# Kernel tuning notes

Hardware: AMD Instinct MI355X
Metric: run time of the kernel (lower is better)

## Reference

```python
import jax, jax.numpy as jnp
import numpy as np

WS = 7  # window size
NH = 3  # num heads
EPS = 1e-5


def _rel_index(ws):
    coords = np.stack(np.meshgrid(np.arange(ws), np.arange(ws), indexing='ij'))  # [2,ws,ws]
    cf = coords.reshape(2, -1)  # [2, ws*ws]
    rel = cf[:, :, None] - cf[:, None, :]  # [2, N, N]
    rel = rel.transpose(1, 2, 0)
    rel[..., 0] += ws - 1
    rel[..., 1] += ws - 1
    rel[..., 0] *= 2 * ws - 1
    return rel.sum(-1).astype(np.int32)  # [N, N]


def setup_inputs() -> dict:
    key = jax.random.key(0)
    ks = jax.random.split(key, 8)
    dim, nh, ws = 96, NH, WS
    hid = 4 * dim
    s = 0.02
    inp = {
        'x': jax.random.normal(ks[0], (16, dim, 224, 224), jnp.float32),
        'ln1_g': jnp.ones((dim,), jnp.float32),
        'ln1_b': jnp.zeros((dim,), jnp.float32),
        'qkv_w': jax.random.normal(ks[1], (dim, 3 * dim), jnp.float32) * s,
        'qkv_b': jnp.zeros((3 * dim,), jnp.float32),
        'rpb_table': jax.random.normal(ks[2], ((2 * ws - 1) ** 2, nh), jnp.float32) * s,
        'proj_w': jax.random.normal(ks[3], (dim, dim), jnp.float32) * s,
        'proj_b': jnp.zeros((dim,), jnp.float32),
        'ln2_g': jnp.ones((dim,), jnp.float32),
        'ln2_b': jnp.zeros((dim,), jnp.float32),
        'mlp_w1': jax.random.normal(ks[4], (dim, hid), jnp.float32) * s,
        'mlp_b1': jnp.zeros((hid,), jnp.float32),
        'mlp_w2': jax.random.normal(ks[5], (hid, dim), jnp.float32) * s,
        'mlp_b2': jnp.zeros((dim,), jnp.float32),
        'rel_index': jnp.asarray(_rel_index(ws)),
    }
    return inp


def _layernorm(x, g, b):
    mu = jnp.mean(x, axis=-1, keepdims=True)
    var = jnp.mean(jnp.square(x - mu), axis=-1, keepdims=True)
    return (x - mu) * jax.lax.rsqrt(var + EPS) * g + b


def reference(x, ln1_g, ln1_b, qkv_w, qkv_b, rpb_table, proj_w, proj_b,
              ln2_g, ln2_b, mlp_w1, mlp_b1, mlp_w2, mlp_b2, rel_index):
    B, C, H, W = x.shape
    ws = WS
    pad_h = (ws - H % ws) % ws
    pad_w = (ws - W % ws) % ws
    x = jnp.transpose(x, (0, 2, 3, 1))  # BHWC
    if pad_h or pad_w:
        x = jnp.pad(x, ((0, 0), (0, pad_h), (0, pad_w), (0, 0)))
    Hp, Wp = H + pad_h, W + pad_w
    shortcut = x
    xn = _layernorm(x, ln1_g, ln1_b)

    # window partition -> [B*nW, N, C]
    N = ws * ws
    xw = xn.reshape(B, Hp // ws, ws, Wp // ws, ws, C)
    xw = jnp.transpose(xw, (0, 1, 3, 2, 4, 5)).reshape(-1, N, C)

    nh = NH
    hd = C // nh
    scale = hd ** -0.5
    qkv = xw @ qkv_w + qkv_b  # [Bw, N, 3C]
    qkv = qkv.reshape(-1, N, 3, nh, hd)
    qkv = jnp.transpose(qkv, (2, 0, 3, 1, 4))  # [3, Bw, nh, N, hd]
    q, k, v = qkv[0], qkv[1], qkv[2]
    attn = jnp.einsum('bhnd,bhmd->bhnm', q * scale, k)
    bias = rpb_table[rel_index.reshape(-1)].reshape(N, N, nh)  # gather
    attn = attn + jnp.transpose(bias, (2, 0, 1))[None]
    attn = jax.nn.softmax(attn, axis=-1)
    out = jnp.einsum('bhnm,bhmd->bhnd', attn, v)
    out = jnp.transpose(out, (0, 2, 1, 3)).reshape(-1, N, C)
    out = out @ proj_w + proj_b

    # window reverse
    xr = out.reshape(B, Hp // ws, Wp // ws, ws, ws, C)
    xr = jnp.transpose(xr, (0, 1, 3, 2, 4, 5)).reshape(B, Hp, Wp, C)

    x = shortcut + xr
    h = _layernorm(x, ln2_g, ln2_b)
    h = jax.nn.gelu(h @ mlp_w1 + mlp_b1, approximate=False) @ mlp_w2 + mlp_b2
    x = x + h
    x = jnp.transpose(x, (0, 3, 1, 2))  # BCHW
    if pad_h or pad_w:
        x = x[:, :, :H, :W]
    return x
```

## Files before the change

### kernel.cpp

```cpp
#include <hip/hip_runtime.h>
#include <math.h>

constexpr int C96  = 96;
constexpr int HW   = 50176;
constexpr int W224 = 224;
constexpr int QKVN = 288;
constexpr int HID  = 384;

typedef __bf16 bf16x8 __attribute__((ext_vector_type(8)));
typedef float  f32x4  __attribute__((ext_vector_type(4)));
typedef unsigned short u16x8 __attribute__((ext_vector_type(8)));

__device__ __forceinline__ float bf2f(unsigned short u) {
    return __uint_as_float(((unsigned int)u) << 16);
}
__device__ __forceinline__ unsigned short f2bf(float f) {
    unsigned int u = __float_as_uint(f);
    u = (u + 0x7fffu + ((u >> 16) & 1u)) >> 16;
    return (unsigned short)u;
}

__device__ __forceinline__ void zero_acc(f32x4 acc[2][3]) {
#pragma unroll
    for (int a = 0; a < 2; ++a)
#pragma unroll
        for (int b = 0; b < 3; ++b)
#pragma unroll
            for (int r = 0; r < 4; ++r) acc[a][b][r] = 0.f;
}

__device__ __forceinline__ void mfma_tile_96(const unsigned short* la, const unsigned short* lb,
                                             int wm, int wn, int l15, int quad,
                                             f32x4 acc[2][3]) {
#pragma unroll
    for (int ks = 0; ks < 3; ++ks) {
        bf16x8 a0 = *(const bf16x8*)&la[(wm*32 +      l15)*104 + ks*32 + quad*8];
        bf16x8 a1 = *(const bf16x8*)&la[(wm*32 + 16 + l15)*104 + ks*32 + quad*8];
#pragma unroll
        for (int fn = 0; fn < 3; ++fn) {
            bf16x8 bv = *(const bf16x8*)&lb[(wn*48 + fn*16 + l15)*104 + ks*32 + quad*8];
            acc[0][fn] = __builtin_amdgcn_mfma_f32_16x16x32_bf16(a0, bv, acc[0][fn], 0, 0, 0);
            acc[1][fn] = __builtin_amdgcn_mfma_f32_16x16x32_bf16(a1, bv, acc[1][fn], 0, 0, 0);
        }
    }
}

__device__ __forceinline__ void ln_rows(unsigned short* la, int tid,
                                        const float* __restrict__ g,
                                        const float* __restrict__ be) {
    const int r  = tid >> 2;
    const int c0 = (tid & 3) * 24;
    float rv[24];
    float s = 0.f;
#pragma unroll
    for (int c = 0; c < 24; ++c) { rv[c] = bf2f(la[r*104 + c0 + c]); s += rv[c]; }
    s += __shfl_xor(s, 1);
    s += __shfl_xor(s, 2);
    const float mu = s * (1.f/96.f);
    float v2 = 0.f;
#pragma unroll
    for (int c = 0; c < 24; ++c) { const float d = rv[c] - mu; v2 += d*d; }
    v2 += __shfl_xor(v2, 1);
    v2 += __shfl_xor(v2, 2);
    const float rs = rsqrtf(v2 * (1.f/96.f) + 1e-5f);
#pragma unroll
    for (int c = 0; c < 24; ++c) {
        la[r*104 + c0 + c] = f2bf((rv[c] - mu) * rs * g[c0 + c] + be[c0 + c]);
    }
}

__global__ __launch_bounds__(256) void k_qkv(const float* __restrict__ x,
                                             const float* __restrict__ g,
                                             const float* __restrict__ be,
                                             const float* __restrict__ w,
                                             const float* __restrict__ bias,
                                             unsigned short* __restrict__ qkv) {
    __shared__ __attribute__((aligned(16))) unsigned short la[64*104];
    __shared__ __attribute__((aligned(16))) unsigned short lb[96*104];
    const int tid   = threadIdx.x;
    const int ncol0 = blockIdx.x * 96;
    const int row0  = blockIdx.y * 64;
    const int b     = row0 / HW;
    const int hw0   = row0 - b*HW;

    for (int idx = tid; idx < 96*16; idx += 256) {
        int c = idx >> 4, t4 = (idx & 15) * 4;
        f32x4 v = *(const f32x4*)&x[(size_t)(b*C96 + c)*HW + hw0 + t4];
#pragma unroll
        for (int e = 0; e < 4; ++e) la[(t4+e)*104 + c] = f2bf(v[e]);
    }
    for (int idx = tid; idx < 96*24; idx += 256) {
        int k = idx / 24, n4 = (idx - k*24) * 4;
        f32x4 v = *(const f32x4*)&w[(size_t)k*QKVN + ncol0 + n4];
#pragma unroll
        for (int e = 0; e < 4; ++e) lb[(n4+e)*104 + k] = f2bf(v[e]);
    }
    __syncthreads();
    ln_rows(la, tid, g, be);
    __syncthreads();

    f32x4 acc[2][3];
    zero_acc(acc);
    const int lane = tid & 63, wv = tid >> 6;
    const int wm = wv & 1, wn = wv >> 1;
    const int l15 = lane & 15, quad = lane >> 4;
    mfma_tile_96(la, lb, wm, wn, l15, quad, acc);

    float bs[3];
#pragma unroll
    for (int fn = 0; fn < 3; ++fn) bs[fn] = bias[ncol0 + wn*48 + fn*16 + l15];
#pragma unroll
    for (int fm = 0; fm < 2; ++fm)
#pragma unroll
        for (int fn = 0; fn < 3; ++fn)
#pragma unroll
            for (int r = 0; r < 4; ++r) {
                int row = row0 + wm*32 + fm*16 + quad*4 + r;
                int col = ncol0 + wn*48 + fn*16 + l15;
                qkv[(size_t)row*QKVN + col] = f2bf(acc[fm][fn][r] + bs[fn]);
            }
}

__global__ __launch_bounds__(256) void k_attn(const unsigned short* __restrict__ qkv,
                                              const float* __restrict__ rpb,
                                              const int* __restrict__ rel,
                                              unsigned short* __restrict__ attn_out) {
    __shared__ __attribute__((aligned(16))) unsigned short lq[49*296];
    __shared__ float ls[3*49*49];
    const int tid = threadIdx.x;
    const int win = blockIdx.x;
    const int b  = win >> 10;
    const int wr = win & 1023;
    const int wh = wr >> 5, ww = wr & 31;
    const int base_hw = (wh*7)*W224 + ww*7;

    for (int idx = tid; idx < 49*36; idx += 256) {
        int i = idx / 36, c8 = (idx - i*36) * 8;
        int row = b*HW + base_hw + (i/7)*W224 + (i - (i/7)*7);
        *(u16x8*)&lq[i*296 + c8] = *(const u16x8*)&qkv[(size_t)row*QKVN + c8];
    }
    __syncthreads();

    const float scale = 0.17677669529663687f;
    for (int idx = tid; idx < 3*49*49; idx += 256) {
        int h  = idx / 2401;
        int r2 = idx - h*2401;
        int i  = r2 / 49, j = r2 - i*49;
        float s = 0.f;
#pragma unroll
        for (int d8 = 0; d8 < 32; d8 += 8) {
            u16x8 qv = *(const u16x8*)&lq[i*296 +       h*32 + d8];
            u16x8 kv = *(const u16x8*)&lq[j*296 +  96 + h*32 + d8];
#pragma unroll
            for (int e = 0; e < 8; ++e) s += bf2f(qv[e]) * bf2f(kv[e]);
        }
        s = s * scale + rpb[rel[r2]*3 + h];
        ls[idx] = s;
    }
    __syncthreads();
    for (int row = tid; row < 147; row += 256) {
        float* p = &ls[row*49];
        float mx = p[0];
        for (int j = 1; j < 49; ++j) mx = fmaxf(mx, p[j]);
        float sm = 0.f;
        for (int j = 0; j < 49; ++j) { float e = __expf(p[j] - mx); p[j] = e; sm += e; }
        float inv = 1.f / sm;
        for (int j = 0; j < 49; ++j) p[j] *= inv;
    }
    __syncthreads();
    for (int idx = tid; idx < 3*49*4; idx += 256) {
        int h  = idx / 196;
        int r2 = idx - h*196;
        int i  = r2 >> 2;
        int d0 = (r2 & 3) * 8;
        const float* sp = &ls[h*2401 + i*49];
        float s[8];
#pragma unroll
        for (int e = 0; e < 8; ++e) s[e] = 0.f;
        for (int j = 0; j < 49; ++j) {
            u16x8 vv = *(const u16x8*)&lq[j*296 + 192 + h*32 + d0];
            float p = sp[j];
#pragma unroll
            for (int e = 0; e < 8; ++e) s[e] += p * bf2f(vv[e]);
        }
        int row = b*HW + base_hw + (i/7)*W224 + (i - (i/7)*7);
        u16x8 res;
#pragma unroll
        for (int e = 0; e < 8; ++e) res[e] = f2bf(s[e]);
        *(u16x8*)&attn_out[(size_t)row*C96 + h*32 + d0] = res;
    }
}

__global__ __launch_bounds__(256) void k_proj(const unsigned short* __restrict__ ain,
                                              const float* __restrict__ w,
                                              const float* __restrict__ bias,
                                              const float* __restrict__ x,
                                              float* __restrict__ x2) {
    __shared__ __attribute__((aligned(16))) unsigned short la[64*104];
    __shared__ __attribute__((aligned(16))) unsigned short lb[96*104];
    const int tid  = threadIdx.x;
    const int row0 = blockIdx.x * 64;
    const int b    = row0 / HW;
    const int hw0  = row0 - b*HW;

    for (int idx = tid; idx < 64*12; idx += 256) {
        int i = idx / 12, c8 = (idx - i*12) * 8;
        *(u16x8*)&la[i*104 + c8] = *(const u16x8*)&ain[(size_t)(row0+i)*C96 + c8];
    }
    for (int idx = tid; idx < 96*24; idx += 256) {
        int k = idx / 24, n4 = (idx - k*24) * 4;
        f32x4 v = *(const f32x4*)&w[(size_t)k*C96 + n4];
#pragma unroll
        for (int e = 0; e < 4; ++e) lb[(n4+e)*104 + k] = f2bf(v[e]);
    }
    __syncthreads();

    f32x4 acc[2][3];
    zero_acc(acc);
    const int lane = tid & 63, wv = tid >> 6;
    const int wm = wv & 1, wn = wv >> 1;
    const int l15 = lane & 15, quad = lane >> 4;
    mfma_tile_96(la, lb, wm, wn, l15, quad, acc);

    float bs[3];
#pragma unroll
    for (int fn = 0; fn < 3; ++fn) bs[fn] = bias[wn*48 + fn*16 + l15];
#pragma unroll
    for (int fm = 0; fm < 2; ++fm)
#pragma unroll
        for (int fn = 0; fn < 3; ++fn)
#pragma unroll
            for (int r = 0; r < 4; ++r) {
                int i   = wm*32 + fm*16 + quad*4 + r;
                int col = wn*48 + fn*16 + l15;
                float v = acc[fm][fn][r] + bs[fn]
                        + x[(size_t)(b*C96 + col)*HW + hw0 + i];
                x2[(size_t)(row0+i)*C96 + col] = v;
            }
}

__global__ __launch_bounds__(256) void k_mlp1(const float* __restrict__ x2,
                                              const float* __restrict__ g,
                                              const float* __restrict__ be,
                                              const float* __restrict__ w,
                                              const float* __restrict__ bias,
                                              unsigned short* __restrict__ hbuf) {
    __shared__ __attribute__((aligned(16))) unsigned short la[64*104];
    __shared__ __attribute__((aligned(16))) unsigned short lb[96*104];
    const int tid   = threadIdx.x;
    const int ncol0 = blockIdx.x * 96;
    const int row0  = blockIdx.y * 64;

    for (int idx = tid; idx < 64*24; idx += 256) {
        int i = idx / 24, c4 = (idx - i*24) * 4;
        f32x4 v = *(const f32x4*)&x2[(size_t)(row0+i)*C96 + c4];
#pragma unroll
        for (int e = 0; e < 4; ++e) la[i*104 + c4 + e] = f2bf(v[e]);
    }
    for (int idx = tid; idx < 96*24; idx += 256) {
        int k = idx / 24, n4 = (idx - k*24) * 4;
        f32x4 v = *(const f32x4*)&w[(size_t)k*HID + ncol0 + n4];
#pragma unroll
        for (int e = 0; e < 4; ++e) lb[(n4+e)*104 + k] = f2bf(v[e]);
    }
    __syncthreads();
    ln_rows(la, tid, g, be);
    __syncthreads();

    f32x4 acc[2][3];
    zero_acc(acc);
    const int lane = tid & 63, wv = tid >> 6;
    const int wm = wv & 1, wn = wv >> 1;
    const int l15 = lane & 15, quad = lane >> 4;
    mfma_tile_96(la, lb, wm, wn, l15, quad, acc);

    float bs[3];
#pragma unroll
    for (int fn = 0; fn < 3; ++fn) bs[fn] = bias[ncol0 + wn*48 + fn*16 + l15];
#pragma unroll
    for (int fm = 0; fm < 2; ++fm)
#pragma unroll
        for (int fn = 0; fn < 3; ++fn)
#pragma unroll
            for (int r = 0; r < 4; ++r) {
                int row = row0 + wm*32 + fm*16 + quad*4 + r;
                int col = ncol0 + wn*48 + fn*16 + l15;
                float v = acc[fm][fn][r] + bs[fn];
                v = 0.5f * v * (1.f + erff(v * 0.70710678118654752f));
                hbuf[(size_t)row*HID + col] = f2bf(v);
            }
}

__global__ __launch_bounds__(256) void k_mlp2(const unsigned short* __restrict__ hbuf,
                                              const float* __restrict__ w,
                                              const float* __restrict__ bias,
                                              const float* __restrict__ x2,
                                              float* __restrict__ out) {
    __shared__ __attribute__((aligned(16))) char smem[(64 + 96) * 104 * 2];
    unsigned short* la = (unsigned short*)smem;
    unsigned short* lb = (unsigned short*)(smem + 64*104*2);
    const int tid  = threadIdx.x;
    const int row0 = blockIdx.x * 64;
    const int b    = row0 / HW;
    const int hw0  = row0 - b*HW;

    f32x4 acc[2][3];
    zero_acc(acc);
    const int lane = tid & 63, wv = tid >> 6;
    const int wm = wv & 1, wn = wv >> 1;
    const int l15 = lane & 15, quad = lane >> 4;

    for (int kb = 0; kb < 4; ++kb) {
        if (kb) __syncthreads();
        for (int idx = tid; idx < 64*12; idx += 256) {
            int i = idx / 12, c8 = (idx - i*12) * 8;
            *(u16x8*)&la[i*104 + c8] =
                *(const u16x8*)&hbuf[(size_t)(row0+i)*HID + kb*96 + c8];
        }
        for (int idx = tid; idx < 96*24; idx += 256) {
            int k = idx / 24, n4 = (idx - k*24) * 4;
            f32x4 v = *(const f32x4*)&w[(size_t)(kb*96 + k)*C96 + n4];
#pragma unroll
            for (int e = 0; e < 4; ++e) lb[(n4+e)*104 + k] = f2bf(v[e]);
        }
        __syncthreads();
        mfma_tile_96(la, lb, wm, wn, l15, quad, acc);
    }
    __syncthreads();

    float* lf = (float*)smem;
    float bs[3];
#pragma unroll
    for (int fn = 0; fn < 3; ++fn) bs[fn] = bias[wn*48 + fn*16 + l15];
#pragma unroll
    for (int fm = 0; fm < 2; ++fm)
#pragma unroll
        for (int fn = 0; fn < 3; ++fn)
#pragma unroll
            for (int r = 0; r < 4; ++r) {
                int i   = wm*32 + fm*16 + quad*4 + r;
                int col = wn*48 + fn*16 + l15;
                lf[i*100 + col] = acc[fm][fn][r] + bs[fn]
                                + x2[(size_t)(row0+i)*C96 + col];
            }
    __syncthreads();
    for (int idx = tid; idx < 96*16; idx += 256) {
        int c = idx >> 4, t4 = (idx & 15) * 4;
        f32x4 v;
#pragma unroll
        for (int e = 0; e < 4; ++e) v[e] = lf[(t4+e)*100 + c];
        *(f32x4*)&out[(size_t)(b*C96 + c)*HW + hw0 + t4] = v;
    }
}

extern "C" void kernel_launch(void* const* d_in, const int* in_sizes, int n_in,
                              void* d_out, int out_size, void* d_ws, size_t ws_size,
                              hipStream_t stream) {
    (void)in_sizes; (void)n_in; (void)out_size;
    const float* x      = (const float*)d_in[0];
    const float* ln1_g  = (const float*)d_in[1];
    const float* ln1_b  = (const float*)d_in[2];
    const float* qkv_w  = (const float*)d_in[3];
    const float* qkv_b  = (const float*)d_in[4];
    const float* rpb    = (const float*)d_in[5];
    const float* proj_w = (const float*)d_in[6];
    const float* proj_b = (const float*)d_in[7];
    const float* ln2_g  = (const float*)d_in[8];
    const float* ln2_b  = (const float*)d_in[9];
    const float* mlp_w1 = (const float*)d_in[10];
    const float* mlp_b1 = (const float*)d_in[11];
    const float* mlp_w2 = (const float*)d_in[12];
    const float* mlp_b2 = (const float*)d_in[13];
    const int*   rel    = (const int*)d_in[14];
    float* out = (float*)d_out;

    constexpr size_t R0 = (size_t)HW * HID * 2;
    constexpr size_t R1 = (size_t)HW * C96 * 2;
    constexpr size_t R2 = (size_t)HW * C96 * 4;
    constexpr size_t PER_IMG = R0 + R1 + R2;

    int nimg = (int)(ws_size / PER_IMG);
    if (nimg < 1)  nimg = 1;
    if (nimg > 16) nimg = 16;

    char* ws = (char*)d_ws;
    unsigned short* qkvb  = (unsigned short*)ws;
    unsigned short* attnb = (unsigned short*)(ws + (size_t)nimg * R0);
    float*          x2b   = (float*)(ws + (size_t)nimg * (R0 + R1));

    for (int c0 = 0; c0 < 16; c0 += nimg) {
        int m = 16 - c0 < nimg ? 16 - c0 : nimg;
        const float* xc = x + (size_t)c0 * C96 * HW;
        float* outc = out + (size_t)c0 * C96 * HW;
        const int MBc = m * (HW / 64);

        k_qkv <<<dim3(3, MBc), 256, 0, stream>>>(xc, ln1_g, ln1_b, qkv_w, qkv_b, qkvb);
        k_attn<<<m * 1024,     256, 0, stream>>>(qkvb, rpb, rel, attnb);
        k_proj<<<MBc,          256, 0, stream>>>(attnb, proj_w, proj_b, xc, x2b);
        k_mlp1<<<dim3(4, MBc), 256, 0, stream>>>(x2b, ln2_g, ln2_b, mlp_w1, mlp_b1, qkvb);
        k_mlp2<<<MBc,          256, 0, stream>>>(qkvb, mlp_w2, mlp_b2, x2b, outc);
    }
}
```

Before: 3.100 ms.

## Rewrite window attention with bf16 MFMA, one wave per window-head

The attention kernel is restructured so each wave handles one window for one head, with four windows per block. QK^T and PV are computed with 16x16x32 bf16 MFMA instructions instead of scalar dot products, and softmax runs in registers using cross-lane shuffles. The relative position bias is pre-gathered into LDS as bf16, and V is stored transposed and zero-padded to fit the MFMA tiles. In exchange, probabilities and bias are rounded to bf16, the 49 tokens are padded to 64, and each block rebuilds the bias table for its head.

```diff
diff --git a/kernel.cpp b/kernel.cpp
--- a/kernel.cpp
+++ b/kernel.cpp
@@ -10,6 +10,7 @@
 typedef __bf16 bf16x8 __attribute__((ext_vector_type(8)));
 typedef float  f32x4  __attribute__((ext_vector_type(4)));
 typedef unsigned short u16x8 __attribute__((ext_vector_type(8)));
+typedef unsigned short u16x4 __attribute__((ext_vector_type(4)));
 
 __device__ __forceinline__ float bf2f(unsigned short u) {
     return __uint_as_float(((unsigned int)u) << 16);
@@ -125,69 +126,140 @@
                                               const float* __restrict__ rpb,
                                               const int* __restrict__ rel,
                                               unsigned short* __restrict__ attn_out) {
-    __shared__ __attribute__((aligned(16))) unsigned short lq[49*296];
-    __shared__ float ls[3*49*49];
-    const int tid = threadIdx.x;
-    const int win = blockIdx.x;
-    const int b  = win >> 10;
-    const int wr = win & 1023;
-    const int wh = wr >> 5, ww = wr & 31;
-    const int base_hw = (wh*7)*W224 + ww*7;
-
-    for (int idx = tid; idx < 49*36; idx += 256) {
-        int i = idx / 36, c8 = (idx - i*36) * 8;
+    __shared__ __attribute__((aligned(16))) unsigned short sm[4*7424 + 2600];
+    const int tid  = threadIdx.x;
+    const int lane = tid & 63;
+    const int wave = tid >> 6;
+    const int h    = blockIdx.x % 3;
+    const int g    = blockIdx.x / 3;
+    const int w    = g*4 + wave;
+    const int b    = w >> 10;
+    const int wr   = w & 1023;
+    const int base_hw = (wr >> 5)*7*W224 + (wr & 31)*7;
+
+    unsigned short* lw = sm + wave*7424;
+    unsigned short* bI = sm + 4*7424;
+
+    for (int idx = tid; idx < 2401; idx += 256) {
+        int i = idx / 49, j = idx - i*49;
+        bI[i*52 + j] = f2bf(rpb[rel[idx]*3 + h]);
+    }
+    for (int idx = lane; idx < 588; idx += 64) {
+        int i = idx / 12, p = idx - i*12;
+        int seg = p >> 2, part = p & 3;
         int row = b*HW + base_hw + (i/7)*W224 + (i - (i/7)*7);
-        *(u16x8*)&lq[i*296 + c8] = *(const u16x8*)&qkv[(size_t)row*QKVN + c8];
-    }
-    __syncthreads();
+        u16x8 v = *(const u16x8*)&qkv[(size_t)row*QKVN + seg*96 + h*32 + part*8];
+        if (seg == 0)      *(u16x8*)&lw[i*40 + part*8] = v;
+        else if (seg == 1) *(u16x8*)&lw[2560 + i*40 + part*8] = v;
+        else {
+            int d0 = part*8;
+#pragma unroll
+            for (int e = 0; e < 8; ++e) lw[5120 + (d0+e)*72 + i] = v[e];
+        }
+    }
+    for (int idx = lane; idx < 480; idx += 64) {
+        int d = idx / 15, j = 49 + (idx - d*15);
+        lw[5120 + d*72 + j] = 0;
+    }
+    __syncthreads();
+
+    const int l15 = lane & 15, quad = lane >> 4;
+
+    f32x4 acc[4][4];
+#pragma unroll
+    for (int mt = 0; mt < 4; ++mt)
+#pragma unroll
+        for (int nt = 0; nt < 4; ++nt)
+#pragma unroll
+            for (int r = 0; r < 4; ++r) acc[mt][nt][r] = 0.f;
+#pragma unroll
+    for (int mt = 0; mt < 4; ++mt) {
+        bf16x8 ak = *(const bf16x8*)&lw[2560 + (mt*16 + l15)*40 + quad*8];
+#pragma unroll
+        for (int nt = 0; nt < 4; ++nt) {
+            bf16x8 bq = *(const bf16x8*)&lw[(nt*16 + l15)*40 + quad*8];
+            acc[mt][nt] = __builtin_amdgcn_mfma_f32_16x16x32_bf16(ak, bq, acc[mt][nt], 0, 0, 0);
+        }
+    }
 
     const float scale = 0.17677669529663687f;
-    for (int idx = tid; idx < 3*49*49; idx += 256) {
-        int h  = idx / 2401;
-        int r2 = idx - h*2401;
-        int i  = r2 / 49, j = r2 - i*49;
-        float s = 0.f;
-#pragma unroll
-        for (int d8 = 0; d8 < 32; d8 += 8) {
-            u16x8 qv = *(const u16x8*)&lq[i*296 +       h*32 + d8];
-            u16x8 kv = *(const u16x8*)&lq[j*296 +  96 + h*32 + d8];
-#pragma unroll
-            for (int e = 0; e < 8; ++e) s += bf2f(qv[e]) * bf2f(kv[e]);
-        }
-        s = s * scale + rpb[rel[r2]*3 + h];
-        ls[idx] = s;
-    }
-    __syncthreads();
-    for (int row = tid; row < 147; row += 256) {
-        float* p = &ls[row*49];
-        float mx = p[0];
-        for (int j = 1; j < 49; ++j) mx = fmaxf(mx, p[j]);
-        float sm = 0.f;
-        for (int j = 0; j < 49; ++j) { float e = __expf(p[j] - mx); p[j] = e; sm += e; }
-        float inv = 1.f / sm;
-        for (int j = 0; j < 49; ++j) p[j] *= inv;
-    }
-    __syncthreads();
-    for (int idx = tid; idx < 3*49*4; idx += 256) {
-        int h  = idx / 196;
-        int r2 = idx - h*196;
-        int i  = r2 >> 2;
-        int d0 = (r2 & 3) * 8;
-        const float* sp = &ls[h*2401 + i*49];
-        float s[8];
-#pragma unroll
-        for (int e = 0; e < 8; ++e) s[e] = 0.f;
-        for (int j = 0; j < 49; ++j) {
-            u16x8 vv = *(const u16x8*)&lq[j*296 + 192 + h*32 + d0];
-            float p = sp[j];
-#pragma unroll
-            for (int e = 0; e < 8; ++e) s[e] += p * bf2f(vv[e]);
-        }
-        int row = b*HW + base_hw + (i/7)*W224 + (i - (i/7)*7);
-        u16x8 res;
-#pragma unroll
-        for (int e = 0; e < 8; ++e) res[e] = f2bf(s[e]);
-        *(u16x8*)&attn_out[(size_t)row*C96 + h*32 + d0] = res;
+#pragma unroll
+    for (int nt = 0; nt < 4; ++nt) {
+        const int ii = nt*16 + l15;
+        const int ib = ii < 49 ? ii : 48;
+        float sv[4][4];
+        float mx = -1e30f;
+#pragma unroll
+        for (int mt = 0; mt < 4; ++mt) {
+            u16x4 bb = *(const u16x4*)&bI[ib*52 + mt*16 + quad*4];
+#pragma unroll
+            for (int r = 0; r < 4; ++r) {
+                int j = mt*16 + quad*4 + r;
+                float v = acc[mt][nt][r]*scale + bf2f(bb[r]);
+                v = (j < 49) ? v : -1e30f;
+                sv[mt][r] = v;
+                mx = fmaxf(mx, v);
+            }
+        }
+        mx = fmaxf(mx, __shfl_xor(mx, 16));
+        mx = fmaxf(mx, __shfl_xor(mx, 32));
+        float sum = 0.f;
+#pragma unroll
+        for (int mt = 0; mt < 4; ++mt)
+#pragma unroll
+            for (int r = 0; r < 4; ++r) {
+                float e = __expf(sv[mt][r] - mx);
+                sv[mt][r] = e; sum += e;
+            }
+        sum += __shfl_xor(sum, 16);
+        sum += __shfl_xor(sum, 32);
+        float inv = 1.f / sum;
+#pragma unroll
+        for (int mt = 0; mt < 4; ++mt) {
+            u16x4 pw;
+#pragma unroll
+            for (int r = 0; r < 4; ++r) pw[r] = f2bf(sv[mt][r] * inv);
+            *(u16x4*)&lw[ii*72 + mt*16 + quad*4] = pw;
+        }
+    }
+    __syncthreads();
+
+    f32x4 acc2[2][4];
+#pragma unroll
+    for (int mt = 0; mt < 2; ++mt)
+#pragma unroll
+        for (int nt = 0; nt < 4; ++nt)
+#pragma unroll
+            for (int r = 0; r < 4; ++r) acc2[mt][nt][r] = 0.f;
+#pragma unroll
+    for (int s = 0; s < 2; ++s)
+#pragma unroll
+        for (int mt = 0; mt < 2; ++mt) {
+            bf16x8 av = *(const bf16x8*)&lw[5120 + (mt*16 + l15)*72 + s*32 + quad*8];
+#pragma unroll
+            for (int nt = 0; nt < 4; ++nt) {
+                bf16x8 bp = *(const bf16x8*)&lw[(nt*16 + l15)*72 + s*32 + quad*8];
+                acc2[mt][nt] = __builtin_amdgcn_mfma_f32_16x16x32_bf16(av, bp, acc2[mt][nt], 0, 0, 0);
+            }
+        }
+    __syncthreads();
+
+#pragma unroll
+    for (int mt = 0; mt < 2; ++mt)
+#pragma unroll
+        for (int nt = 0; nt < 4; ++nt) {
+            int ii = nt*16 + l15;
+            u16x4 o4;
+#pragma unroll
+            for (int r = 0; r < 4; ++r) o4[r] = f2bf(acc2[mt][nt][r]);
+            *(u16x4*)&lw[ii*40 + mt*16 + quad*4] = o4;
+        }
+    __syncthreads();
+
+    for (int idx = lane; idx < 196; idx += 64) {
+        int t = idx >> 2, c8 = (idx & 3)*8;
+        int row = b*HW + base_hw + (t/7)*W224 + (t - (t/7)*7);
+        *(u16x8*)&attn_out[(size_t)row*C96 + h*32 + c8] = *(const u16x8*)&lw[t*40 + c8];
     }
 }
 
@@ -395,7 +467,7 @@
         const int MBc = m * (HW / 64);
 
         k_qkv <<<dim3(3, MBc), 256, 0, stream>>>(xc, ln1_g, ln1_b, qkv_w, qkv_b, qkvb);
-        k_attn<<<m * 1024,     256, 0, stream>>>(qkvb, rpb, rel, attnb);
+        k_attn<<<m * 768,      256, 0, stream>>>(qkvb, rpb, rel, attnb);
         k_proj<<<MBc,          256, 0, stream>>>(attnb, proj_w, proj_b, xc, x2b);
         k_mlp1<<<dim3(4, MBc), 256, 0, stream>>>(x2b, ln2_g, ln2_b, mlp_w1, mlp_b1, qkvb);
         k_mlp2<<<MBc,          256, 0, stream>>>(qkvb, mlp_w2, mlp_b2, x2b, outc);
```

Measured after the change: 2.647 ms. -14.6%, faster.
